# Kernel optimization log

Measured on AMD Instinct MI355X. Metric: run time of the kernel, lower is better.

Reference implementation:

```python
import jax, jax.numpy as jnp
import numpy as np
import jax.scipy.special as jsp

N_RESERVOIR = 8192
N_INPUT = 64
N_LAYERS = 3
INPUT_SCALE = 0.4
RES_SCALE = 0.9
BIAS_SCALE = 0.1
ALPHA = 1.0  # activation_fn_args = (1.0,)
N_HADAMARD = 1 << int(np.ceil(np.log2(N_INPUT + N_RESERVOIR)))  # 16384
N_PADDING = N_HADAMARD - N_RESERVOIR - N_INPUT
BATCH = 512


def fwht(x):
    """Fast Walsh-Hadamard transform along last axis. x: [B, n], n a power of 2."""
    B, n = x.shape
    h = 1
    while h < n:
        x = x.reshape(B, n // (2 * h), 2, h)
        a = x[:, :, 0, :]
        b = x[:, :, 1, :]
        x = jnp.concatenate([a + b, a - b], axis=-1).reshape(B, n)
        h *= 2
    return x


def leaky_erf(x, state, alpha):
    return (1.0 - alpha) * state + alpha * jsp.erf(x)


def setup_inputs() -> dict:
    key = jax.random.key(0)
    k1, k2, k3, k4 = jax.random.split(key, 4)
    state = jax.random.normal(k1, (BATCH, N_RESERVOIR), dtype=jnp.float32)
    inputs = jax.random.normal(k2, (BATCH, N_INPUT), dtype=jnp.float32)
    bias = BIAS_SCALE * jax.random.normal(k3, (N_RESERVOIR,), dtype=jnp.float32)
    # structured-transform diagonals: random Rademacher signs, one per layer
    diag = jnp.where(jax.random.uniform(k4, (N_LAYERS, N_HADAMARD)) < 0.5, -1.0, 1.0).astype(jnp.float32)
    return {"state": state, "inputs": inputs, "bias": bias, "diag": diag}


def reference(state, inputs, bias, diag):
    B = state.shape[0]
    pad = jnp.zeros((B, N_PADDING), dtype=state.dtype)
    X = jnp.concatenate([RES_SCALE * state, INPUT_SCALE * inputs, pad], axis=1)  # [B, N_HADAMARD]
    for l in range(N_LAYERS):
        X = fwht(X * diag[l])
    z = X[:, :N_RESERVOIR] / N_HADAMARD + bias
    return leaky_erf(z, state, ALPHA)
```

## Files before the change

### kernel.cpp

```cpp
#include <hip/hip_runtime.h>
#include <math.h>

#define NH    16384
#define NRES  8192
#define NINP  64
#define BATCH 512

typedef float v2f __attribute__((ext_vector_type(2)));

__device__ __forceinline__ constexpr int gfold(int v) {
    return ((v >> 5) & 7) ^ ((v >> 8) & 7) ^ ((v >> 11) & 7);
}
__device__ __forceinline__ constexpr int physf(int v) {
    return v ^ (gfold(v) << 2);
}

__device__ __forceinline__ v2f pk_add(v2f a, v2f b) {
    v2f d;
    asm("v_pk_add_f32 %0, %1, %2" : "=v"(d) : "v"(a), "v"(b));
    return d;
}
__device__ __forceinline__ v2f pk_sub(v2f a, v2f b, v2f negone) {
    v2f d;
    asm("v_pk_fma_f32 %0, %1, %2, %3" : "=v"(d) : "v"(b), "v"(negone), "v"(a));
    return d;
}

template <int T>
__device__ __forceinline__ void pstage(v2f X[16], v2f negone) {
#pragma unroll
    for (int p = 0; p < 16; ++p) {
        if (!(p & T)) {
            v2f A = X[p], B = X[p | T];
            X[p]     = pk_add(A, B);
            X[p | T] = pk_sub(A, B, negone);
        }
    }
}
__device__ __forceinline__ void vstage0(v2f X[16]) {
#pragma unroll
    for (int p = 0; p < 16; ++p) {
        float a = X[p].x, b = X[p].y;
        X[p].x = a + b;
        X[p].y = a - b;
    }
}
__device__ __forceinline__ void jpass(v2f X[16], v2f negone) {
    pstage<2>(X, negone); pstage<4>(X, negone); pstage<8>(X, negone);
}

template <int CTRL>
__device__ __forceinline__ float dppf(float v) {
    return __builtin_bit_cast(float,
        __builtin_amdgcn_update_dpp(0, __builtin_bit_cast(int, v), CTRL, 0xF, 0xF, true));
}
template <int CTRL>
__device__ __forceinline__ void dpp_swap(float A, float B, bool odd, float& oA, float& oB) {
    float dA = dppf<CTRL>(A), dB = dppf<CTRL>(B);
    oA = odd ? dB : A;
    oB = odd ? B  : dA;
}
__device__ __forceinline__ void pl16_swap(float& a, float& b) {
    asm("v_permlane16_swap_b32 %0, %1" : "+v"(a), "+v"(b));
}
__device__ __forceinline__ void pl32_swap(float& a, float& b) {
    asm("v_permlane32_swap_b32 %0, %1" : "+v"(a), "+v"(b));
}

__device__ __forceinline__ void shuffle_exchange(v2f X[16], bool odd0) {
#pragma unroll
    for (int p = 0; p < 16; ++p) if (!(p & 2)) {
        float a0, a1, b0, b1;
        dpp_swap<0xB1>(X[p].x, X[p | 2].x, odd0, a0, b0);
        dpp_swap<0xB1>(X[p].y, X[p | 2].y, odd0, a1, b1);
        X[p] = (v2f){a0, a1}; X[p | 2] = (v2f){b0, b1};
    }
#pragma unroll
    for (int p = 0; p < 16; ++p) if (!(p & 4)) {
        float a = X[p].x, b = X[p | 4].x; pl16_swap(a, b); X[p].x = a; X[p | 4].x = b;
        float c = X[p].y, d = X[p | 4].y; pl16_swap(c, d); X[p].y = c; X[p | 4].y = d;
    }
#pragma unroll
    for (int p = 0; p < 16; ++p) if (!(p & 8)) {
        float a = X[p].x, b = X[p | 8].x; pl32_swap(a, b); X[p].x = a; X[p | 8].x = b;
        float c = X[p].y, d = X[p | 8].y; pl32_swap(c, d); X[p].y = c; X[p | 8].y = d;
    }
}

#define GOFF(g, G0, G1, G2) \
    (((g) & 1 ? (G0) : 0) | ((g) & 2 ? (G1) : 0) | ((g) & 4 ? (G2) : 0))

#define WRX(Q, G0, G1, G2) do { _Pragma("unroll") \
    for (int g = 0; g < 8; ++g) \
        lds4[(unsigned)((Q) ^ physf(GOFF(g, G0, G1, G2))) >> 2] = \
            make_float4(X[2*g].x, X[2*g].y, X[2*g+1].x, X[2*g+1].y); } while (0)

#define RDX(Q, G0, G1, G2) do { _Pragma("unroll") \
    for (int g = 0; g < 8; ++g) { \
        float4 v = lds4[(unsigned)((Q) ^ physf(GOFF(g, G0, G1, G2))) >> 2]; \
        X[2*g]   = (v2f){v.x, v.y}; \
        X[2*g+1] = (v2f){v.z, v.w}; } } while (0)

#define DIAG_MUL(BASE, G0, G1, G2) do { _Pragma("unroll") \
    for (int h = 0; h < 2; ++h) { \
        float4 dv[4]; \
        _Pragma("unroll") for (int k = 0; k < 4; ++k) \
            dv[k] = *(const float4*)((BASE) + GOFF(h * 4 + k, G0, G1, G2)); \
        _Pragma("unroll") for (int k = 0; k < 4; ++k) { \
            const int g = h * 4 + k; \
            X[2*g]   *= (v2f){dv[k].x, dv[k].y}; \
            X[2*g+1] *= (v2f){dv[k].z, dv[k].w}; \
        } \
    } } while (0)

#define BAR() asm volatile("s_waitcnt lgkmcnt(0)\n\ts_barrier" ::: "memory")

__device__ __forceinline__ float erf_fast(float z) {
    float p = z * z;
    float u = z * fmaf(p, 0.10090f, 1.1283793f);
    float e = __builtin_amdgcn_exp2f(u * 2.8853902f);
    float r = __builtin_amdgcn_rcpf(e + 1.0f);
    return fmaf(-2.0f, r, 1.0f);
}

__global__ __launch_bounds__(512, 2) void st_kernel(
    const float* __restrict__ state, const float* __restrict__ inputs,
    const float* __restrict__ bias,  const float* __restrict__ diag,
    float* __restrict__ out)
{
    __shared__ float4 lds4[NH / 4];
    const int t = threadIdx.x;
    const int r = blockIdx.x;
    const int l = t & 63, w = t >> 6;
    const int l0 = l & 1, l1 = (l >> 1) & 1, l2 = (l >> 2) & 1;
    const int l3 = (l >> 3) & 1, l4 = (l >> 4) & 1, l5 = (l >> 5) & 1;
    const int w0 = w & 1, w1 = (w >> 1) & 1, w2 = (w >> 2) & 1;
    const bool odd0 = l0;

    const int b_w1 = l0*4 + l4*8 + l5*16 + l1*64 + l2*128 + l3*256
                   + w0*2048 + w1*4096 + w2*8192;
    const int b_r1 = w0*4 + w1*8 + w2*16 + l1*32 + l0*64 + l4*128
                   + l5*256 + l2*512 + l3*1024;
    const int b_r2 = l0*32 + w0*64 + w1*128 + w2*256 + l4*512
                   + l5*1024 + l1*2048 + l2*4096 + l3*8192;
    const int b_r3 = l1*4 + l2*8 + l3*16 + w0*32 + w1*512 + w2*1024
                   + l0*2048 + l4*4096 + l5*8192;
    const int b_d1 = w0*4 + w1*8 + w2*16 + l1*32 + l2*512 + l3*1024
                   + l0*2048 + l4*4096 + l5*8192;
    const int b_d2 = l0*4 + l4*8 + l5*16 + w0*64 + w1*128 + w2*256
                   + l1*2048 + l2*4096 + l3*8192;
    const int b_st = l1*4 + l2*8 + l3*16 + w0*32 + l0*64 + l4*128
                   + l5*256 + w1*512 + w2*1024;

    const v2f negone = (v2f){-1.0f, -1.0f};
    v2f X[16];

    if (t < 256) {
        const float* srow = state + (size_t)r * NRES + t * 32;
        const float* d0   = diag + t * 32;
#pragma unroll
        for (int g = 0; g < 8; ++g) {
            float4 v = *(const float4*)(srow + 4 * g);
            float4 d = *(const float4*)(d0 + 4 * g);
            X[2*g]   = (v2f){0.9f * v.x * d.x, 0.9f * v.y * d.y};
            X[2*g+1] = (v2f){0.9f * v.z * d.z, 0.9f * v.w * d.w};
        }
    } else if (t < 258) {
        const float* irow = inputs + r * NINP + (t - 256) * 32;
        const float* d0   = diag + t * 32;
#pragma unroll
        for (int g = 0; g < 8; ++g) {
            float4 v = *(const float4*)(irow + 4 * g);
            float4 d = *(const float4*)(d0 + 4 * g);
            X[2*g]   = (v2f){0.4f * v.x * d.x, 0.4f * v.y * d.y};
            X[2*g+1] = (v2f){0.4f * v.z * d.z, 0.4f * v.w * d.w};
        }
    } else {
#pragma unroll
        for (int p = 0; p < 16; ++p) X[p] = (v2f){0.f, 0.f};
    }

    vstage0(X); pstage<1>(X, negone);
    jpass(X, negone);
    shuffle_exchange(X, odd0);
    jpass(X, negone);

    { const int Q = physf(b_w1); WRX(Q, 32, 512, 1024); }
    BAR();
    { const int Q = physf(b_r1); RDX(Q, 2048, 4096, 8192); }
    jpass(X, negone);
    shuffle_exchange(X, odd0);
    jpass(X, negone);

    DIAG_MUL(diag + NH + b_d1, 64, 128, 256);
    vstage0(X); pstage<1>(X, negone);
    jpass(X, negone);
    shuffle_exchange(X, odd0);
    jpass(X, negone);

    BAR();
    { const int Q = physf(b_r1); WRX(Q, 2048, 4096, 8192); }
    BAR();
    { const int Q = physf(b_r2); RDX(Q, 4, 8, 16); }
    jpass(X, negone);
    shuffle_exchange(X, odd0);
    jpass(X, negone);

    DIAG_MUL(diag + 2 * NH + b_d2, 32, 512, 1024);
    vstage0(X); pstage<1>(X, negone);
    jpass(X, negone);
    shuffle_exchange(X, odd0);
    jpass(X, negone);

    BAR();
    { const int Q = physf(b_r2); WRX(Q, 4, 8, 16); }
    BAR();
    { const int Q = physf(b_r3); RDX(Q, 64, 128, 256); }
    jpass(X, negone);
    shuffle_exchange(X, odd0);
    jpass(X, negone);

    {
        float* orow = out + (size_t)r * NRES;
        const float inv = 1.0f / (float)NH;
#pragma unroll
        for (int g = 0; g < 4; ++g) {
            const int a = b_st + (g & 1) * 2048 + (g >> 1) * 4096;
            float4 b = *(const float4*)(bias + a);
            float4 o;
            o.x = erf_fast(fmaf(X[2*g].x,   inv, b.x));
            o.y = erf_fast(fmaf(X[2*g].y,   inv, b.y));
            o.z = erf_fast(fmaf(X[2*g+1].x, inv, b.z));
            o.w = erf_fast(fmaf(X[2*g+1].y, inv, b.w));
            *(float4*)(orow + a) = o;
        }
    }
}

extern "C" void kernel_launch(void* const* d_in, const int* in_sizes, int n_in,
                              void* d_out, int out_size, void* d_ws, size_t ws_size,
                              hipStream_t stream) {
    (void)in_sizes; (void)n_in; (void)out_size; (void)d_ws; (void)ws_size;
    const float* state  = (const float*)d_in[0];
    const float* inputs = (const float*)d_in[1];
    const float* bias   = (const float*)d_in[2];
    const float* diag   = (const float*)d_in[3];
    float* out = (float*)d_out;

    hipLaunchKernelGGL(st_kernel, dim3(BATCH), dim3(512), 0, stream,
                       state, inputs, bias, diag, out);
}
```

Baseline: 27.07 us.

## Roll three Hadamard layers into a loop with prefetched diagonals and bias

```diff
diff --git a/kernel.cpp b/kernel.cpp
--- a/kernel.cpp
+++ b/kernel.cpp
@@ -8,45 +8,36 @@
 
 typedef float v2f __attribute__((ext_vector_type(2)));
 
-__device__ __forceinline__ constexpr int gfold(int v) {
+__device__ __forceinline__ constexpr int gfoldc(int v) {
     return ((v >> 5) & 7) ^ ((v >> 8) & 7) ^ ((v >> 11) & 7);
 }
-__device__ __forceinline__ constexpr int physf(int v) {
-    return v ^ (gfold(v) << 2);
-}
+__device__ __forceinline__ constexpr int physf(int v) { return v ^ (gfoldc(v) << 2); }
 
 __device__ __forceinline__ v2f pk_add(v2f a, v2f b) {
-    v2f d;
-    asm("v_pk_add_f32 %0, %1, %2" : "=v"(d) : "v"(a), "v"(b));
-    return d;
-}
-__device__ __forceinline__ v2f pk_sub(v2f a, v2f b, v2f negone) {
-    v2f d;
-    asm("v_pk_fma_f32 %0, %1, %2, %3" : "=v"(d) : "v"(b), "v"(negone), "v"(a));
-    return d;
+    v2f d; asm("v_pk_add_f32 %0, %1, %2" : "=v"(d) : "v"(a), "v"(b)); return d;
+}
+__device__ __forceinline__ v2f pk_sub(v2f a, v2f b, v2f n1) {
+    v2f d; asm("v_pk_fma_f32 %0, %1, %2, %3" : "=v"(d) : "v"(b), "v"(n1), "v"(a)); return d;
 }
 
 template <int T>
-__device__ __forceinline__ void pstage(v2f X[16], v2f negone) {
-#pragma unroll
-    for (int p = 0; p < 16; ++p) {
-        if (!(p & T)) {
-            v2f A = X[p], B = X[p | T];
-            X[p]     = pk_add(A, B);
-            X[p | T] = pk_sub(A, B, negone);
-        }
+__device__ __forceinline__ void pstage(v2f X[16], v2f n1) {
+#pragma unroll
+    for (int p = 0; p < 16; ++p) if (!(p & T)) {
+        v2f A = X[p], B = X[p | T];
+        X[p]     = pk_add(A, B);
+        X[p | T] = pk_sub(A, B, n1);
     }
 }
 __device__ __forceinline__ void vstage0(v2f X[16]) {
 #pragma unroll
     for (int p = 0; p < 16; ++p) {
         float a = X[p].x, b = X[p].y;
-        X[p].x = a + b;
-        X[p].y = a - b;
-    }
-}
-__device__ __forceinline__ void jpass(v2f X[16], v2f negone) {
-    pstage<2>(X, negone); pstage<4>(X, negone); pstage<8>(X, negone);
+        X[p].x = a + b; X[p].y = a - b;
+    }
+}
+__device__ __forceinline__ void jpass(v2f X[16], v2f n1) {
+    pstage<2>(X, n1); pstage<4>(X, n1); pstage<8>(X, n1);
 }
 
 template <int CTRL>
@@ -86,32 +77,6 @@
         float c = X[p].y, d = X[p | 8].y; pl32_swap(c, d); X[p].y = c; X[p | 8].y = d;
     }
 }
-
-#define GOFF(g, G0, G1, G2) \
-    (((g) & 1 ? (G0) : 0) | ((g) & 2 ? (G1) : 0) | ((g) & 4 ? (G2) : 0))
-
-#define WRX(Q, G0, G1, G2) do { _Pragma("unroll") \
-    for (int g = 0; g < 8; ++g) \
-        lds4[(unsigned)((Q) ^ physf(GOFF(g, G0, G1, G2))) >> 2] = \
-            make_float4(X[2*g].x, X[2*g].y, X[2*g+1].x, X[2*g+1].y); } while (0)
-
-#define RDX(Q, G0, G1, G2) do { _Pragma("unroll") \
-    for (int g = 0; g < 8; ++g) { \
-        float4 v = lds4[(unsigned)((Q) ^ physf(GOFF(g, G0, G1, G2))) >> 2]; \
-        X[2*g]   = (v2f){v.x, v.y}; \
-        X[2*g+1] = (v2f){v.z, v.w}; } } while (0)
-
-#define DIAG_MUL(BASE, G0, G1, G2) do { _Pragma("unroll") \
-    for (int h = 0; h < 2; ++h) { \
-        float4 dv[4]; \
-        _Pragma("unroll") for (int k = 0; k < 4; ++k) \
-            dv[k] = *(const float4*)((BASE) + GOFF(h * 4 + k, G0, G1, G2)); \
-        _Pragma("unroll") for (int k = 0; k < 4; ++k) { \
-            const int g = h * 4 + k; \
-            X[2*g]   *= (v2f){dv[k].x, dv[k].y}; \
-            X[2*g+1] *= (v2f){dv[k].z, dv[k].w}; \
-        } \
-    } } while (0)
 
 #define BAR() asm volatile("s_waitcnt lgkmcnt(0)\n\ts_barrier" ::: "memory")
 
@@ -132,106 +97,114 @@
     const int t = threadIdx.x;
     const int r = blockIdx.x;
     const int l = t & 63, w = t >> 6;
-    const int l0 = l & 1, l1 = (l >> 1) & 1, l2 = (l >> 2) & 1;
-    const int l3 = (l >> 3) & 1, l4 = (l >> 4) & 1, l5 = (l >> 5) & 1;
-    const int w0 = w & 1, w1 = (w >> 1) & 1, w2 = (w >> 2) & 1;
+    const int l0=l&1, l1=(l>>1)&1, l2=(l>>2)&1, l3=(l>>3)&1, l4=(l>>4)&1, l5=(l>>5)&1;
+    const int w0=w&1, w1=(w>>1)&1, w2=(w>>2)&1;
     const bool odd0 = l0;
 
-    const int b_w1 = l0*4 + l4*8 + l5*16 + l1*64 + l2*128 + l3*256
-                   + w0*2048 + w1*4096 + w2*8192;
-    const int b_r1 = w0*4 + w1*8 + w2*16 + l1*32 + l0*64 + l4*128
-                   + l5*256 + l2*512 + l3*1024;
-    const int b_r2 = l0*32 + w0*64 + w1*128 + w2*256 + l4*512
-                   + l5*1024 + l1*2048 + l2*4096 + l3*8192;
-    const int b_r3 = l1*4 + l2*8 + l3*16 + w0*32 + w1*512 + w2*1024
-                   + l0*2048 + l4*4096 + l5*8192;
-    const int b_d1 = w0*4 + w1*8 + w2*16 + l1*32 + l2*512 + l3*1024
-                   + l0*2048 + l4*4096 + l5*8192;
-    const int b_d2 = l0*4 + l4*8 + l5*16 + w0*64 + w1*128 + w2*256
-                   + l1*2048 + l2*4096 + l3*8192;
-    const int b_st = l1*4 + l2*8 + l3*16 + w0*32 + l0*64 + l4*128
-                   + l5*256 + w1*512 + w2*1024;
-
-    const v2f negone = (v2f){-1.0f, -1.0f};
+    const int b0 = l0*32 + l4*64 + l5*128 + l1*256 + l2*512 + l3*1024
+                 + w0*2048 + w1*4096 + w2*8192;
+    const int b1 = w0*4 + w1*8 + w2*16 + l1*32 + l2*64 + l3*128
+                 + l0*256 + l4*512 + l5*1024;
+    const int bP = l0*4 + l4*8 + l5*16 + l1*256 + l2*512 + l3*1024
+                 + w0*2048 + w1*4096 + w2*8192;
+    const int bR = w0*4 + w1*8 + w2*16 + l1*32 + l2*64 + l3*128
+                 + l0*2048 + l4*4096 + l5*8192;
+
+    int Qw = physf(bP), Qr = physf(bR);
+    int GW0 = 36,  GW1 = 72,  GW2 = 144;
+    int GR0 = 260, GR1 = 520, GR2 = 1040;
+    int dbN = b1, DN0 = 2048, DN1 = 4096, DN2 = 8192;
+    int dbO = b0, DO0 = 4,    DO1 = 8,    DO2 = 16;
+
+    const v2f n1 = (v2f){-1.0f, -1.0f};
     v2f X[16];
+    float4 dv[8];
 
     if (t < 256) {
-        const float* srow = state + (size_t)r * NRES + t * 32;
-        const float* d0   = diag + t * 32;
+        const float* srow = state + (size_t)r * NRES + b0;
 #pragma unroll
         for (int g = 0; g < 8; ++g) {
             float4 v = *(const float4*)(srow + 4 * g);
-            float4 d = *(const float4*)(d0 + 4 * g);
-            X[2*g]   = (v2f){0.9f * v.x * d.x, 0.9f * v.y * d.y};
-            X[2*g+1] = (v2f){0.9f * v.z * d.z, 0.9f * v.w * d.w};
+            X[2*g]   = (v2f){0.9f * v.x, 0.9f * v.y};
+            X[2*g+1] = (v2f){0.9f * v.z, 0.9f * v.w};
         }
     } else if (t < 258) {
-        const float* irow = inputs + r * NINP + (t - 256) * 32;
-        const float* d0   = diag + t * 32;
+        const float* irow = inputs + r * NINP + (b0 - 8192);
 #pragma unroll
         for (int g = 0; g < 8; ++g) {
             float4 v = *(const float4*)(irow + 4 * g);
-            float4 d = *(const float4*)(d0 + 4 * g);
-            X[2*g]   = (v2f){0.4f * v.x * d.x, 0.4f * v.y * d.y};
-            X[2*g+1] = (v2f){0.4f * v.z * d.z, 0.4f * v.w * d.w};
+            X[2*g]   = (v2f){0.4f * v.x, 0.4f * v.y};
+            X[2*g+1] = (v2f){0.4f * v.z, 0.4f * v.w};
         }
     } else {
 #pragma unroll
         for (int p = 0; p < 16; ++p) X[p] = (v2f){0.f, 0.f};
     }
-
-    vstage0(X); pstage<1>(X, negone);
-    jpass(X, negone);
-    shuffle_exchange(X, odd0);
-    jpass(X, negone);
-
-    { const int Q = physf(b_w1); WRX(Q, 32, 512, 1024); }
-    BAR();
-    { const int Q = physf(b_r1); RDX(Q, 2048, 4096, 8192); }
-    jpass(X, negone);
-    shuffle_exchange(X, odd0);
-    jpass(X, negone);
-
-    DIAG_MUL(diag + NH + b_d1, 64, 128, 256);
-    vstage0(X); pstage<1>(X, negone);
-    jpass(X, negone);
-    shuffle_exchange(X, odd0);
-    jpass(X, negone);
-
-    BAR();
-    { const int Q = physf(b_r1); WRX(Q, 2048, 4096, 8192); }
-    BAR();
-    { const int Q = physf(b_r2); RDX(Q, 4, 8, 16); }
-    jpass(X, negone);
-    shuffle_exchange(X, odd0);
-    jpass(X, negone);
-
-    DIAG_MUL(diag + 2 * NH + b_d2, 32, 512, 1024);
-    vstage0(X); pstage<1>(X, negone);
-    jpass(X, negone);
-    shuffle_exchange(X, odd0);
-    jpass(X, negone);
-
-    BAR();
-    { const int Q = physf(b_r2); WRX(Q, 4, 8, 16); }
-    BAR();
-    { const int Q = physf(b_r3); RDX(Q, 64, 128, 256); }
-    jpass(X, negone);
-    shuffle_exchange(X, odd0);
-    jpass(X, negone);
+#pragma unroll
+    for (int g = 0; g < 8; ++g) dv[g] = *(const float4*)(diag + b0 + 4 * g);
+    float4 bv[4];
+#pragma unroll
+    for (int g = 0; g < 4; ++g)
+        bv[g] = *(const float4*)(bias + b1 + (g & 1) * 2048 + (g >> 1) * 4096);
+
+#pragma unroll 1
+    for (int lay = 0; lay < 3; ++lay) {
+#pragma unroll
+        for (int g = 0; g < 8; ++g) {
+            X[2*g]   *= (v2f){dv[g].x, dv[g].y};
+            X[2*g+1] *= (v2f){dv[g].z, dv[g].w};
+        }
+        {
+            const float* dn = diag + (size_t)((lay < 2) ? (lay + 1) : 2) * NH + dbN;
+#pragma unroll
+            for (int g = 0; g < 8; ++g) {
+                const int off = ((g & 1) ? DN0 : 0) + ((g & 2) ? DN1 : 0) + ((g & 4) ? DN2 : 0);
+                dv[g] = *(const float4*)(dn + off);
+            }
+        }
+        vstage0(X); pstage<1>(X, n1);
+        jpass(X, n1);
+        shuffle_exchange(X, odd0);
+        jpass(X, n1);
+        BAR();
+#pragma unroll
+        for (int g = 0; g < 8; ++g) {
+            const int a = Qw ^ ((g & 1) ? GW0 : 0) ^ ((g & 2) ? GW1 : 0) ^ ((g & 4) ? GW2 : 0);
+            lds4[(unsigned)a >> 2] =
+                make_float4(X[2*g].x, X[2*g].y, X[2*g+1].x, X[2*g+1].y);
+        }
+        BAR();
+#pragma unroll
+        for (int g = 0; g < 8; ++g) {
+            const int a = Qr ^ ((g & 1) ? GR0 : 0) ^ ((g & 2) ? GR1 : 0) ^ ((g & 4) ? GR2 : 0);
+            float4 v = lds4[(unsigned)a >> 2];
+            X[2*g]   = (v2f){v.x, v.y};
+            X[2*g+1] = (v2f){v.z, v.w};
+        }
+        jpass(X, n1);
+        shuffle_exchange(X, odd0);
+        jpass(X, n1);
+        { int q = Qw; Qw = Qr; Qr = q; }
+        { int a = GW0; GW0 = GR0; GR0 = a;
+          int b = GW1; GW1 = GR1; GR1 = b;
+          int c = GW2; GW2 = GR2; GR2 = c; }
+        { int a = dbN; dbN = dbO; dbO = a;
+          int x = DN0; DN0 = DO0; DO0 = x;
+          int y = DN1; DN1 = DO1; DO1 = y;
+          int z = DN2; DN2 = DO2; DO2 = z; }
+    }
 
     {
         float* orow = out + (size_t)r * NRES;
         const float inv = 1.0f / (float)NH;
 #pragma unroll
         for (int g = 0; g < 4; ++g) {
-            const int a = b_st + (g & 1) * 2048 + (g >> 1) * 4096;
-            float4 b = *(const float4*)(bias + a);
+            const int a = b1 + (g & 1) * 2048 + (g >> 1) * 4096;
             float4 o;
-            o.x = erf_fast(fmaf(X[2*g].x,   inv, b.x));
-            o.y = erf_fast(fmaf(X[2*g].y,   inv, b.y));
-            o.z = erf_fast(fmaf(X[2*g+1].x, inv, b.z));
-            o.w = erf_fast(fmaf(X[2*g+1].y, inv, b.w));
+            o.x = erf_fast(fmaf(X[2*g].x,   inv, bv[g].x));
+            o.y = erf_fast(fmaf(X[2*g].y,   inv, bv[g].y));
+            o.z = erf_fast(fmaf(X[2*g+1].x, inv, bv[g].z));
+            o.w = erf_fast(fmaf(X[2*g+1].y, inv, bv[g].w));
             *(float4*)(orow + a) = o;
         }
     }
```

New measurement: 40.71 us. 1.5x slower.
